# Performance work log

Hardware: AMD Instinct MI355X
Metric: run time of the kernel (lower is better)

The kernel has to match this reference:

```python
import jax, jax.numpy as jnp
import numpy as np

N = 50000
E = 800000


def _degrees(src, dst):
    ones = jnp.ones((E,), dtype=jnp.float32)
    indeg = jax.ops.segment_sum(ones, dst, num_segments=N)
    outdeg = jax.ops.segment_sum(ones, src, num_segments=N)
    return indeg, outdeg


def _aggregate(h, src, dst):
    # update_all(copy_src, sum): gather src features, scatter-add to dst
    return jax.ops.segment_sum(h[src], dst, num_segments=N)


def _graph_conv(h, src, dst, innorm, outnorm, W, b):
    h = h * outnorm[:, None]
    h = _aggregate(h, src, dst)
    h = h * innorm[:, None]
    return h @ W + b


def setup_inputs() -> dict:
    key = jax.random.key(0)
    ks = jax.random.split(key, 8)
    d_in, d_hid, d_out = 128, 128, 64
    inp = {
        "features": jax.random.normal(ks[0], (N, d_in), dtype=jnp.float32),
        "src": jax.random.randint(ks[1], (E,), 0, N, dtype=jnp.int32),
        "dst": jax.random.randint(ks[2], (E,), 0, N, dtype=jnp.int32),
        "W0": jax.random.normal(ks[3], (d_in, d_hid), dtype=jnp.float32) / np.sqrt(d_in),
        "b0": jnp.zeros((d_hid,), dtype=jnp.float32),
        "W1": jax.random.normal(ks[4], (d_hid, d_hid), dtype=jnp.float32) / np.sqrt(d_hid),
        "b1": jnp.zeros((d_hid,), dtype=jnp.float32),
        "W2": jax.random.normal(ks[5], (d_hid, d_hid), dtype=jnp.float32) / np.sqrt(d_hid),
        "b2": jnp.zeros((d_hid,), dtype=jnp.float32),
        "W3": jax.random.normal(ks[6], (d_hid, d_out), dtype=jnp.float32) / np.sqrt(d_hid),
        "b3": jnp.zeros((d_out,), dtype=jnp.float32),
    }
    return inp


def reference(features, src, dst, W0, b0, W1, b1, W2, b2, W3, b3):
    indeg, outdeg = _degrees(src, dst)
    innorm = jnp.power(jnp.clip(indeg, 1.0, None), -0.5)
    outnorm = jnp.power(jnp.clip(outdeg, 1.0, None), -0.5)

    # input GraphConv + relu
    h = jax.nn.relu(_graph_conv(features, src, dst, innorm, outnorm, W0, b0))

    # GResConv blocks: graph_res=True, raw_res=True, dropout=0 (identity)
    for (W, b) in ((W1, b1), (W2, b2)):
        res = features * innorm[:, None]          # pre-norm (in-degree)
        res = _aggregate(res, src, dst)
        res = res * innorm[:, None]               # post-norm (in-degree)
        h = jax.nn.relu(_graph_conv(h, src, dst, innorm, outnorm, W, b) + res)

    # output GraphConv (no activation)
    return _graph_conv(h, src, dst, innorm, outnorm, W3, b3)
```

## Files before the change

### kernel.cpp

```cpp
#include <hip/hip_runtime.h>


#define GN 50000
#define GE 800000
#define SCAN_CHUNK 1024
#define DEG_BLOCKS 128
#define DEG_SLICE 6250
#define HALF_NODES 25000
#define HALF_WORDS 12500

typedef __attribute__((ext_vector_type(8))) short bf16x8;
typedef __attribute__((ext_vector_type(4))) float f32x4;

__device__ __forceinline__ float u2f(unsigned int u) { return __uint_as_float(u); }

__device__ __forceinline__ unsigned int bfr(float a) {
  unsigned int u = __float_as_uint(a);
  return (u + 0x7fffu + ((u >> 16) & 1u)) >> 16;
}
__device__ __forceinline__ unsigned int bfpack(float a, float b) {
  return bfr(a) | (bfr(b) << 16);
}
__device__ __forceinline__ void bfunpack8(uint4 u, float* f) {
  f[0] = u2f(u.x << 16); f[1] = u2f(u.x & 0xffff0000u);
  f[2] = u2f(u.y << 16); f[3] = u2f(u.y & 0xffff0000u);
  f[4] = u2f(u.z << 16); f[5] = u2f(u.z & 0xffff0000u);
  f[6] = u2f(u.w << 16); f[7] = u2f(u.w & 0xffff0000u);
}

__global__ __launch_bounds__(512) void degrees_lds_kernel(
    const int* __restrict__ src, const int* __restrict__ dst,
    unsigned int* __restrict__ partials, int E) {
  __shared__ unsigned int hist[HALF_WORDS];
  for (int i = threadIdx.x; i < HALF_WORDS; i += 512) hist[i] = 0u;
  __syncthreads();
  int b    = blockIdx.x & 127;
  int half = (blockIdx.x >> 7) & 1;
  int dir  = blockIdx.x >> 8;
  const int* __restrict__ idx = dir ? src : dst;
  int lo = half * HALF_NODES, hi = lo + HALF_NODES;
  int s = b * DEG_SLICE;
  int e = min(s + DEG_SLICE, E);
  for (int i = s + threadIdx.x; i < e; i += 512) {
    int node = idx[i];
    if (node >= lo && node < hi) {
      int local = node - lo;
      atomicAdd(&hist[local >> 1], 1u << ((local & 1) << 4));
    }
  }
  __syncthreads();
  unsigned int* outp = partials + (((size_t)dir * 2 + half) * DEG_BLOCKS + b) * HALF_WORDS;
  for (int i = threadIdx.x; i < HALF_WORDS; i += 512) outp[i] = hist[i];
}

__global__ void degrees_reduce_kernel(const unsigned int* __restrict__ partials,
                                      int* __restrict__ indeg, float* __restrict__ innorm,
                                      float* __restrict__ outnorm, float2* __restrict__ nrm2,
                                      unsigned int* __restrict__ rel16pk) {
  int g = blockIdx.x * blockDim.x + threadIdx.x;
  if (g >= 2 * HALF_WORDS) return;
  int half = (g >= HALF_WORDS) ? 1 : 0;
  int w = g - half * HALF_WORDS;
  int n0 = half * HALF_NODES + 2 * w;
  unsigned int inLo = 0, inHi = 0, outLo = 0, outHi = 0;
  const unsigned int* pIn  = partials + ((size_t)(0 * 2 + half) * DEG_BLOCKS) * HALF_WORDS + w;
  const unsigned int* pOut = partials + ((size_t)(1 * 2 + half) * DEG_BLOCKS) * HALF_WORDS + w;
#pragma unroll 4
  for (int b = 0; b < DEG_BLOCKS; b++) {
    rel16pk[((size_t)b * GN + n0) >> 1] = inLo | (inHi << 16);
    unsigned int v = pIn[(size_t)b * HALF_WORDS];
    inLo += v & 0xffffu; inHi += v >> 16;
    unsigned int u = pOut[(size_t)b * HALF_WORDS];
    outLo += u & 0xffffu; outHi += u >> 16;
  }
  indeg[n0]     = (int)inLo;
  indeg[n0 + 1] = (int)inHi;
  float i0 = rsqrtf((float)max((int)inLo, 1)),  i1 = rsqrtf((float)max((int)inHi, 1));
  float o0 = rsqrtf((float)max((int)outLo, 1)), o1 = rsqrtf((float)max((int)outHi, 1));
  innorm[n0] = i0; innorm[n0 + 1] = i1;
  outnorm[n0] = o0; outnorm[n0 + 1] = o1;
  nrm2[n0]     = make_float2(o0, i0);
  nrm2[n0 + 1] = make_float2(o1, i1);
}

__global__ __launch_bounds__(256) void scan_blocksums(const int* __restrict__ deg,
                                                      int* __restrict__ bsums, int n) {
  int tid = threadIdx.x;
  int i = blockIdx.x * SCAN_CHUNK + tid * 4;
  int s = 0;
  if (i + 3 < n) {
    int4 v = *(const int4*)(deg + i);
    s = v.x + v.y + v.z + v.w;
  } else {
    for (int j = 0; j < 4; j++) if (i + j < n) s += deg[i + j];
  }
  for (int off = 32; off; off >>= 1) s += __shfl_down(s, off);
  __shared__ int ws[4];
  if ((tid & 63) == 0) ws[tid >> 6] = s;
  __syncthreads();
  if (tid == 0) bsums[blockIdx.x] = ws[0] + ws[1] + ws[2] + ws[3];
}

__global__ void scan_bsums(const int* __restrict__ bsums, int* __restrict__ bpref,
                           int nb, int* __restrict__ offsets, int n) {
  int tid = threadIdx.x;
  int v = (tid < nb) ? bsums[tid] : 0;
  int incl = v;
  for (int off = 1; off < 64; off <<= 1) {
    int t = __shfl_up(incl, off);
    if (tid >= off) incl += t;
  }
  if (tid < nb) bpref[tid] = incl - v;
  if (tid == 63) offsets[n] = incl;
}

__global__ __launch_bounds__(256) void scan_final(const int* __restrict__ deg,
                                                  const int* __restrict__ bpref,
                                                  int* __restrict__ offsets, int n) {
  int tid = threadIdx.x;
  int i = blockIdx.x * SCAN_CHUNK + tid * 4;
  int v[4];
#pragma unroll
  for (int j = 0; j < 4; j++) v[j] = (i + j < n) ? deg[i + j] : 0;
  int tsum = v[0] + v[1] + v[2] + v[3];
  int incl = tsum;
  for (int off = 1; off < 64; off <<= 1) {
    int t = __shfl_up(incl, off);
    if ((tid & 63) >= off) incl += t;
  }
  __shared__ int wsum[4];
  int wid = tid >> 6, lane = tid & 63;
  if (lane == 63) wsum[wid] = incl;
  __syncthreads();
  int wpref = 0;
  for (int w = 0; w < wid; w++) wpref += wsum[w];
  int run = bpref[blockIdx.x] + wpref + incl - tsum;
#pragma unroll
  for (int j = 0; j < 4; j++) {
    if (i + j < n) offsets[i + j] = run;
    run += v[j];
  }
}

__global__ __launch_bounds__(512) void fill_csr_lds_kernel(
    const int* __restrict__ src, const int* __restrict__ dst,
    const int* __restrict__ offsets, const unsigned short* __restrict__ rel16,
    const float2* __restrict__ nrm2, int* __restrict__ csr,
    float2* __restrict__ esc2, int E) {
  __shared__ unsigned int cnt[HALF_WORDS];
  for (int i = threadIdx.x; i < HALF_WORDS; i += 512) cnt[i] = 0u;
  __syncthreads();
  int b    = blockIdx.x & 127;
  int half = blockIdx.x >> 7;
  int lo = half * HALF_NODES, hi = lo + HALF_NODES;
  int s = b * DEG_SLICE;
  int e = min(s + DEG_SLICE, E);
  const unsigned short* relb = rel16 + (size_t)b * GN;
  for (int i = s + threadIdx.x; i < e; i += 512) {
    int d = dst[i];
    if (d >= lo && d < hi) {
      int local = d - lo;
      int sh = (local & 1) << 4;
      unsigned int old = atomicAdd(&cnt[local >> 1], 1u << sh);
      int rank = (int)((old >> sh) & 0xffffu);
      int pos = offsets[d] + (int)relb[d] + rank;
      int sv = src[i];
      csr[pos] = sv;
      esc2[pos] = nrm2[sv];
    }
  }
}

__global__ __launch_bounds__(256) void f32_to_bf16_kernel(const float* __restrict__ in,
                                                          uint4* __restrict__ out, int n8) {
  int t = blockIdx.x * blockDim.x + threadIdx.x;
  if (t >= n8) return;
  const float4* in4 = (const float4*)in;
  float4 f0 = in4[2 * t], f1 = in4[2 * t + 1];
  uint4 o;
  o.x = bfpack(f0.x, f0.y); o.y = bfpack(f0.z, f0.w);
  o.z = bfpack(f1.x, f1.y); o.w = bfpack(f1.z, f1.w);
  out[t] = o;
}

__global__ __launch_bounds__(256) void wconvert_kernel(
    const float* __restrict__ W0, const float* __restrict__ W1,
    const float* __restrict__ W2, const float* __restrict__ W3,
    unsigned short* __restrict__ wt) {
  int e = blockIdx.x * 256 + threadIdx.x;
  if (e >= 3 * 16384 + 8192) return;
  int m, local, N;
  if (e < 49152) { m = e >> 14; local = e & 16383; N = 128; }
  else { m = 3; local = e - 49152; N = 64; }
  const float* W = (m == 0) ? W0 : (m == 1) ? W1 : (m == 2) ? W2 : W3;
  int k = local / N, n = local % N;
  float v = W[k * N + n];
  unsigned int hi = bfr(v);
  float rem = v - u2f(hi << 16);
  unsigned int lo = bfr(rem);
  size_t hibase = (m < 3) ? (size_t)m * 32768 : 98304;
  size_t lobase = hibase + ((m < 3) ? 16384 : 8192);
  wt[hibase + (size_t)n * 128 + k] = (unsigned short)hi;
  wt[lobase + (size_t)n * 128 + k] = (unsigned short)lo;
}

__global__ __launch_bounds__(256) void aggregate128_bf16_kernel(
    const char* __restrict__ hqc, const float2* __restrict__ esc2,
    const float* __restrict__ wscale, const int* __restrict__ offsets,
    const int* __restrict__ csr, uint4* __restrict__ outq, int n) {
  int node = blockIdx.x * 4 + (threadIdx.x >> 6);
  if (node >= n) return;
  int lane = threadIdx.x & 63;
  unsigned cofs = (unsigned)(lane & 15) << 4;
  int p = lane >> 4;
  int s = offsets[node], e = offsets[node + 1];
  float acc[8];
#pragma unroll
  for (int j = 0; j < 8; j++) acc[j] = 0.f;
  int i = s + p;
  for (; i + 4 < e; i += 8) {
    int sn0 = csr[i], sn1 = csr[i + 4];
    float s0 = esc2[i].x, s1 = esc2[i + 4].x;
    uint4 u0 = *(const uint4*)(hqc + (((unsigned)sn0 << 8) + cofs));
    uint4 u1 = *(const uint4*)(hqc + (((unsigned)sn1 << 8) + cofs));
    float f0[8], f1[8];
    bfunpack8(u0, f0); bfunpack8(u1, f1);
#pragma unroll
    for (int j = 0; j < 8; j++) acc[j] += f0[j] * s0 + f1[j] * s1;
  }
  if (i < e) {
    int sn = csr[i];
    float sc = esc2[i].x;
    uint4 u = *(const uint4*)(hqc + (((unsigned)sn << 8) + cofs));
    float f[8]; bfunpack8(u, f);
#pragma unroll
    for (int j = 0; j < 8; j++) acc[j] += f[j] * sc;
  }
#pragma unroll
  for (int off = 32; off >= 16; off >>= 1)
#pragma unroll
    for (int j = 0; j < 8; j++) acc[j] += __shfl_down(acc[j], off);
  if (lane < 16) {
    float w = wscale[node];
    uint4 q;
    q.x = bfpack(acc[0] * w, acc[1] * w); q.y = bfpack(acc[2] * w, acc[3] * w);
    q.z = bfpack(acc[4] * w, acc[5] * w); q.w = bfpack(acc[6] * w, acc[7] * w);
    outq[(size_t)node * 16 + (lane & 15)] = q;
  }
}

__global__ __launch_bounds__(256) void aggregate_dual_bf16_kernel(
    const char* __restrict__ hqc, const float2* __restrict__ esc2,
    const float* __restrict__ wscale, const int* __restrict__ offsets,
    const int* __restrict__ csr, uint4* __restrict__ out1q,
    uint4* __restrict__ out2q, int n) {
  int node = blockIdx.x * 4 + (threadIdx.x >> 6);
  if (node >= n) return;
  int lane = threadIdx.x & 63;
  unsigned cofs = (unsigned)(lane & 15) << 4;
  int p = lane >> 4;
  int s = offsets[node], e = offsets[node + 1];
  float a1[8], a2[8];
#pragma unroll
  for (int j = 0; j < 8; j++) { a1[j] = 0.f; a2[j] = 0.f; }
  int i = s + p;
  for (; i + 4 < e; i += 8) {
    int sn0 = csr[i], sn1 = csr[i + 4];
    float2 g0 = esc2[i], g1 = esc2[i + 4];
    uint4 u0 = *(const uint4*)(hqc + (((unsigned)sn0 << 8) + cofs));
    uint4 u1 = *(const uint4*)(hqc + (((unsigned)sn1 << 8) + cofs));
    float f0[8], f1[8];
    bfunpack8(u0, f0); bfunpack8(u1, f1);
#pragma unroll
    for (int j = 0; j < 8; j++) {
      a1[j] += f0[j] * g0.x + f1[j] * g1.x;
      a2[j] += f0[j] * g0.y + f1[j] * g1.y;
    }
  }
  if (i < e) {
    int sn = csr[i];
    float2 g = esc2[i];
    uint4 u = *(const uint4*)(hqc + (((unsigned)sn << 8) + cofs));
    float f[8]; bfunpack8(u, f);
#pragma unroll
    for (int j = 0; j < 8; j++) { a1[j] += f[j] * g.x; a2[j] += f[j] * g.y; }
  }
#pragma unroll
  for (int off = 32; off >= 16; off >>= 1)
#pragma unroll
    for (int j = 0; j < 8; j++) {
      a1[j] += __shfl_down(a1[j], off);
      a2[j] += __shfl_down(a2[j], off);
    }
  if (lane < 16) {
    float w = wscale[node];
    uint4 q1, q2;
    q1.x = bfpack(a1[0] * w, a1[1] * w); q1.y = bfpack(a1[2] * w, a1[3] * w);
    q1.z = bfpack(a1[4] * w, a1[5] * w); q1.w = bfpack(a1[6] * w, a1[7] * w);
    q2.x = bfpack(a2[0] * w, a2[1] * w); q2.y = bfpack(a2[2] * w, a2[3] * w);
    q2.z = bfpack(a2[4] * w, a2[5] * w); q2.w = bfpack(a2[6] * w, a2[7] * w);
    out1q[(size_t)node * 16 + (lane & 15)] = q1;
    out2q[(size_t)node * 16 + (lane & 15)] = q2;
  }
}

__global__ __launch_bounds__(256) void aggregate64_bf16_kernel(
    const char* __restrict__ hqc, const float2* __restrict__ esc2,
    const float* __restrict__ wscale, const float* __restrict__ bias,
    const int* __restrict__ offsets, const int* __restrict__ csr,
    float* __restrict__ out, int n) {
  int node = blockIdx.x * 4 + (threadIdx.x >> 6);
  if (node >= n) return;
  int lane = threadIdx.x & 63;
  unsigned cofs = (unsigned)(lane & 7) << 4;
  int p = lane >> 3;
  int s = offsets[node], e = offsets[node + 1];
  float acc[8];
#pragma unroll
  for (int j = 0; j < 8; j++) acc[j] = 0.f;
  int i = s + p;
  for (; i + 8 < e; i += 16) {
    int sn0 = csr[i], sn1 = csr[i + 8];
    float s0 = esc2[i].x, s1 = esc2[i + 8].x;
    uint4 u0 = *(const uint4*)(hqc + (((unsigned)sn0 << 7) + cofs));
    uint4 u1 = *(const uint4*)(hqc + (((unsigned)sn1 << 7) + cofs));
    float f0[8], f1[8];
    bfunpack8(u0, f0); bfunpack8(u1, f1);
#pragma unroll
    for (int j = 0; j < 8; j++) acc[j] += f0[j] * s0 + f1[j] * s1;
  }
  if (i < e) {
    int sn = csr[i];
    float sc = esc2[i].x;
    uint4 u = *(const uint4*)(hqc + (((unsigned)sn << 7) + cofs));
    float f[8]; bfunpack8(u, f);
#pragma unroll
    for (int j = 0; j < 8; j++) acc[j] += f[j] * sc;
  }
#pragma unroll
  for (int off = 32; off >= 8; off >>= 1)
#pragma unroll
    for (int j = 0; j < 8; j++) acc[j] += __shfl_down(acc[j], off);
  if (lane < 8) {
    int c = lane;
    float w = wscale[node];
    const float4* bp = (const float4*)bias;
    float4 b0 = bp[2 * c], b1 = bp[2 * c + 1];
    float4* orow = (float4*)(out + (size_t)node * 64);
    orow[2 * c]     = make_float4(acc[0] * w + b0.x, acc[1] * w + b0.y,
                                  acc[2] * w + b0.z, acc[3] * w + b0.w);
    orow[2 * c + 1] = make_float4(acc[4] * w + b1.x, acc[5] * w + b1.y,
                                  acc[6] * w + b1.z, acc[7] * w + b1.w);
  }
}

template <int NT, bool RELU, bool HAS_BIAS, bool ADD_RES>
__global__ __launch_bounds__(256) void mfma_gemm_kernel(
    const unsigned short* __restrict__ Abf, const unsigned short* __restrict__ Wth,
    const unsigned short* __restrict__ Wtl, const float* __restrict__ bias,
    const unsigned short* __restrict__ resbf, unsigned short* __restrict__ outbf, int M) {
  constexpr int DOUT = NT * 16;
  int wid = threadIdx.x >> 6, lane = threadIdx.x & 63;
  int row0 = (blockIdx.x * 4 + wid) * 32;
  int lr = lane & 15, g = lane >> 4;
  bf16x8 a[2][4];
  bf16x8 zz = {0, 0, 0, 0, 0, 0, 0, 0};
#pragma unroll
  for (int rt = 0; rt < 2; rt++) {
    int r = row0 + rt * 16 + lr;
    if (r < M) {
      const unsigned short* ap = Abf + (size_t)r * 128 + g * 8;
#pragma unroll
      for (int s = 0; s < 4; s++) a[rt][s] = *(const bf16x8*)(ap + s * 32);
    } else {
#pragma unroll
      for (int s = 0; s < 4; s++) a[rt][s] = zz;
    }
  }
#pragma unroll
  for (int ct = 0; ct < NT; ct++) {
    const unsigned short* wph = Wth + (size_t)(ct * 16 + lr) * 128 + g * 8;
    const unsigned short* wpl = Wtl + (size_t)(ct * 16 + lr) * 128 + g * 8;
    bf16x8 wh[4], wl[4];
#pragma unroll
    for (int s = 0; s < 4; s++) {
      wh[s] = *(const bf16x8*)(wph + s * 32);
      wl[s] = *(const bf16x8*)(wpl + s * 32);
    }
    f32x4 acc0 = {0.f, 0.f, 0.f, 0.f}, acc1 = {0.f, 0.f, 0.f, 0.f};
#pragma unroll
    for (int s = 0; s < 4; s++) {
      acc0 = __builtin_amdgcn_mfma_f32_16x16x32_bf16(a[0][s], wh[s], acc0, 0, 0, 0);
      acc0 = __builtin_amdgcn_mfma_f32_16x16x32_bf16(a[0][s], wl[s], acc0, 0, 0, 0);
      acc1 = __builtin_amdgcn_mfma_f32_16x16x32_bf16(a[1][s], wh[s], acc1, 0, 0, 0);
      acc1 = __builtin_amdgcn_mfma_f32_16x16x32_bf16(a[1][s], wl[s], acc1, 0, 0, 0);
    }
    int col = ct * 16 + lr;
    float bv = HAS_BIAS ? bias[col] : 0.f;
#pragma unroll
    for (int rt = 0; rt < 2; rt++) {
      f32x4 acc = rt ? acc1 : acc0;
#pragma unroll
      for (int j = 0; j < 4; j++) {
        int r = row0 + rt * 16 + g * 4 + j;
        if (r < M) {
          float v = acc[j] + bv;
          if (ADD_RES) v += u2f((unsigned int)resbf[(size_t)r * 128 + col] << 16);
          if (RELU) v = fmaxf(v, 0.f);
          outbf[(size_t)r * DOUT + col] = (unsigned short)bfr(v);
        }
      }
    }
  }
}

extern "C" void kernel_launch(void* const* d_in, const int* in_sizes, int n_in,
                              void* d_out, int out_size, void* d_ws, size_t ws_size,
                              hipStream_t stream) {
  const float* features = (const float*)d_in[0];
  const int*   src      = (const int*)d_in[1];
  const int*   dst      = (const int*)d_in[2];
  const float* W0 = (const float*)d_in[3];
  const float* b0 = (const float*)d_in[4];
  const float* W1 = (const float*)d_in[5];
  const float* b1 = (const float*)d_in[6];
  const float* W2 = (const float*)d_in[7];
  const float* b2 = (const float*)d_in[8];
  const float* W3 = (const float*)d_in[9];
  const float* b3 = (const float*)d_in[10];
  float* out = (float*)d_out;
  const int N = GN, E = GE;

  char* ws = (char*)d_ws;
  size_t off = 0;
  auto alloc = [&](size_t bytes) -> void* {
    void* p = ws + off;
    off = (off + bytes + 255) & ~(size_t)255;
    return p;
  };
  unsigned int* partials = (unsigned int*)alloc((size_t)2 * 2 * DEG_BLOCKS * HALF_WORDS * 4);
  unsigned int* rel16pk  = (unsigned int*)alloc((size_t)DEG_BLOCKS * GN * 2);
  int*   indeg   = (int*)alloc((size_t)N * 4);
  float* innorm  = (float*)alloc((size_t)N * 4);
  float* outnorm = (float*)alloc((size_t)N * 4);
  float2* nrm2   = (float2*)alloc((size_t)N * 8);
  int*   offsets = (int*)alloc((size_t)(N + 1) * 4);
  int*   csr     = (int*)alloc((size_t)E * 4);
  float2* esc2   = (float2*)alloc((size_t)E * 8);
  int*   bsums   = (int*)alloc((size_t)256 * 4);
  int*   bpref   = (int*)alloc((size_t)256 * 4);
  unsigned short* wt = (unsigned short*)alloc((size_t)114688 * 2);
  uint4* fbf = (uint4*)alloc((size_t)N * 128 * 2);
  unsigned short* resbf = (unsigned short*)alloc((size_t)N * 128 * 2);
  unsigned short* tbf = (unsigned short*)alloc((size_t)N * 128 * 2);
  unsigned short* hbf = (unsigned short*)alloc((size_t)N * 128 * 2);
  (void)ws_size; (void)in_sizes; (void)n_in; (void)out_size;

  unsigned short* Ybf = resbf;
  const unsigned short *w0h = wt,          *w0l = wt + 16384;
  const unsigned short *w1h = wt + 32768,  *w1l = wt + 49152;
  const unsigned short *w2h = wt + 65536,  *w2l = wt + 81920;
  const unsigned short *w3h = wt + 98304,  *w3l = wt + 106496;

  degrees_lds_kernel<<<4 * DEG_BLOCKS, 512, 0, stream>>>(src, dst, partials, E);
  degrees_reduce_kernel<<<(2 * HALF_WORDS + 255) / 256, 256, 0, stream>>>(
      partials, indeg, innorm, outnorm, nrm2, rel16pk);

  int nb = (N + SCAN_CHUNK - 1) / SCAN_CHUNK;
  scan_blocksums<<<nb, 256, 0, stream>>>(indeg, bsums, N);
  scan_bsums<<<1, 64, 0, stream>>>(bsums, bpref, nb, offsets, N);
  scan_final<<<nb, 256, 0, stream>>>(indeg, bpref, offsets, N);

  fill_csr_lds_kernel<<<2 * DEG_BLOCKS, 512, 0, stream>>>(
      src, dst, offsets, (const unsigned short*)rel16pk, nrm2, csr, esc2, E);

  wconvert_kernel<<<(57344 + 255) / 256, 256, 0, stream>>>(W0, W1, W2, W3, wt);
  f32_to_bf16_kernel<<<(N * 128 / 8 + 255) / 256, 256, 0, stream>>>(
      features, fbf, N * 128 / 8);

  int aggGrid  = (N + 3) / 4;
  int gemmGrid = (N + 127) / 128;

  aggregate_dual_bf16_kernel<<<aggGrid, 256, 0, stream>>>(
      (const char*)fbf, esc2, innorm, offsets, csr, (uint4*)tbf, (uint4*)resbf, N);
  mfma_gemm_kernel<8, true, true, false><<<gemmGrid, 256, 0, stream>>>(
      tbf, w0h, w0l, b0, nullptr, hbf, N);
  aggregate128_bf16_kernel<<<aggGrid, 256, 0, stream>>>(
      (const char*)hbf, esc2, innorm, offsets, csr, (uint4*)tbf, N);
  mfma_gemm_kernel<8, true, true, true><<<gemmGrid, 256, 0, stream>>>(
      tbf, w1h, w1l, b1, resbf, hbf, N);
  aggregate128_bf16_kernel<<<aggGrid, 256, 0, stream>>>(
      (const char*)hbf, esc2, innorm, offsets, csr, (uint4*)tbf, N);
  mfma_gemm_kernel<8, true, true, true><<<gemmGrid, 256, 0, stream>>>(
      tbf, w2h, w2l, b2, resbf, hbf, N);
  mfma_gemm_kernel<4, false, false, false><<<gemmGrid, 256, 0, stream>>>(
      hbf, w3h, w3l, nullptr, nullptr, Ybf, N);
  aggregate64_bf16_kernel<<<aggGrid, 256, 0, stream>>>(
      (const char*)Ybf, esc2, innorm, b3, offsets, csr, out, N);
}
```

Baseline: 373.8 us.

## Merge scan and convert kernels, split GEMM columns over grid, halve degree blocks

Folds the single-block bsums scan into scan_final and merges the feature and weight bf16 conversions into one launch, removing two kernel launches. The MFMA GEMM now splits output columns across a second grid dimension, swaps operand order so each lane writes four contiguous columns with vectorized bias, residual and output accesses, and keeps separate hi/lo accumulators. Degree and CSR-fill kernels use 64 larger slices instead of 128, shrinking the partials and rel16 buffers, and the unused outnorm array is dropped. The trade-offs are redundant per-block scans of bsums, fewer blocks in the histogram stages, and extra accumulator registers in the GEMM.

```diff
diff --git a/kernel.cpp b/kernel.cpp
--- a/kernel.cpp
+++ b/kernel.cpp
@@ -4,8 +4,8 @@
 #define GN 50000
 #define GE 800000
 #define SCAN_CHUNK 1024
-#define DEG_BLOCKS 128
-#define DEG_SLICE 6250
+#define DEG_BLOCKS 64
+#define DEG_SLICE 12500
 #define HALF_NODES 25000
 #define HALF_WORDS 12500
 
@@ -34,9 +34,9 @@
   __shared__ unsigned int hist[HALF_WORDS];
   for (int i = threadIdx.x; i < HALF_WORDS; i += 512) hist[i] = 0u;
   __syncthreads();
-  int b    = blockIdx.x & 127;
-  int half = (blockIdx.x >> 7) & 1;
-  int dir  = blockIdx.x >> 8;
+  int b    = blockIdx.x & 63;
+  int half = (blockIdx.x >> 6) & 1;
+  int dir  = blockIdx.x >> 7;
   const int* __restrict__ idx = dir ? src : dst;
   int lo = half * HALF_NODES, hi = lo + HALF_NODES;
   int s = b * DEG_SLICE;
@@ -55,7 +55,7 @@
 
 __global__ void degrees_reduce_kernel(const unsigned int* __restrict__ partials,
                                       int* __restrict__ indeg, float* __restrict__ innorm,
-                                      float* __restrict__ outnorm, float2* __restrict__ nrm2,
+                                      float2* __restrict__ nrm2,
                                       unsigned int* __restrict__ rel16pk) {
   int g = blockIdx.x * blockDim.x + threadIdx.x;
   if (g >= 2 * HALF_WORDS) return;
@@ -78,7 +78,6 @@
   float i0 = rsqrtf((float)max((int)inLo, 1)),  i1 = rsqrtf((float)max((int)inHi, 1));
   float o0 = rsqrtf((float)max((int)outLo, 1)), o1 = rsqrtf((float)max((int)outHi, 1));
   innorm[n0] = i0; innorm[n0 + 1] = i1;
-  outnorm[n0] = o0; outnorm[n0 + 1] = o1;
   nrm2[n0]     = make_float2(o0, i0);
   nrm2[n0 + 1] = make_float2(o1, i1);
 }
@@ -101,23 +100,22 @@
   if (tid == 0) bsums[blockIdx.x] = ws[0] + ws[1] + ws[2] + ws[3];
 }
 
-__global__ void scan_bsums(const int* __restrict__ bsums, int* __restrict__ bpref,
-                           int nb, int* __restrict__ offsets, int n) {
+__global__ __launch_bounds__(256) void scan_final(const int* __restrict__ deg,
+                                                  const int* __restrict__ bsums, int nb,
+                                                  int* __restrict__ offsets, int n) {
+  __shared__ int bpref_s, total_s;
   int tid = threadIdx.x;
-  int v = (tid < nb) ? bsums[tid] : 0;
-  int incl = v;
-  for (int off = 1; off < 64; off <<= 1) {
-    int t = __shfl_up(incl, off);
-    if (tid >= off) incl += t;
-  }
-  if (tid < nb) bpref[tid] = incl - v;
-  if (tid == 63) offsets[n] = incl;
-}
-
-__global__ __launch_bounds__(256) void scan_final(const int* __restrict__ deg,
-                                                  const int* __restrict__ bpref,
-                                                  int* __restrict__ offsets, int n) {
-  int tid = threadIdx.x;
+  if (tid < 64) {
+    int v = (tid < nb) ? bsums[tid] : 0;
+    int incl = v;
+    for (int off = 1; off < 64; off <<= 1) {
+      int t = __shfl_up(incl, off);
+      if (tid >= off) incl += t;
+    }
+    if (tid == (int)blockIdx.x) bpref_s = incl - v;
+    if (tid == nb - 1) total_s = incl;
+  }
+  __syncthreads();
   int i = blockIdx.x * SCAN_CHUNK + tid * 4;
   int v[4];
 #pragma unroll
@@ -134,12 +132,13 @@
   __syncthreads();
   int wpref = 0;
   for (int w = 0; w < wid; w++) wpref += wsum[w];
-  int run = bpref[blockIdx.x] + wpref + incl - tsum;
+  int run = bpref_s + wpref + incl - tsum;
 #pragma unroll
   for (int j = 0; j < 4; j++) {
     if (i + j < n) offsets[i + j] = run;
     run += v[j];
   }
+  if (blockIdx.x == 0 && tid == 0) offsets[n] = total_s;
 }
 
 __global__ __launch_bounds__(512) void fill_csr_lds_kernel(
@@ -150,8 +149,8 @@
   __shared__ unsigned int cnt[HALF_WORDS];
   for (int i = threadIdx.x; i < HALF_WORDS; i += 512) cnt[i] = 0u;
   __syncthreads();
-  int b    = blockIdx.x & 127;
-  int half = blockIdx.x >> 7;
+  int b    = blockIdx.x & 63;
+  int half = blockIdx.x >> 6;
   int lo = half * HALF_NODES, hi = lo + HALF_NODES;
   int s = b * DEG_SLICE;
   int e = min(s + DEG_SLICE, E);
@@ -171,23 +170,23 @@
   }
 }
 
-__global__ __launch_bounds__(256) void f32_to_bf16_kernel(const float* __restrict__ in,
-                                                          uint4* __restrict__ out, int n8) {
-  int t = blockIdx.x * blockDim.x + threadIdx.x;
-  if (t >= n8) return;
-  const float4* in4 = (const float4*)in;
-  float4 f0 = in4[2 * t], f1 = in4[2 * t + 1];
-  uint4 o;
-  o.x = bfpack(f0.x, f0.y); o.y = bfpack(f0.z, f0.w);
-  o.z = bfpack(f1.x, f1.y); o.w = bfpack(f1.z, f1.w);
-  out[t] = o;
-}
-
-__global__ __launch_bounds__(256) void wconvert_kernel(
+#define FB_BLOCKS 3125
+__global__ __launch_bounds__(256) void convert_kernel(
+    const float* __restrict__ fin, uint4* __restrict__ fbf,
     const float* __restrict__ W0, const float* __restrict__ W1,
     const float* __restrict__ W2, const float* __restrict__ W3,
     unsigned short* __restrict__ wt) {
-  int e = blockIdx.x * 256 + threadIdx.x;
+  if ((int)blockIdx.x < FB_BLOCKS) {
+    int t = blockIdx.x * 256 + threadIdx.x;
+    const float4* in4 = (const float4*)fin;
+    float4 f0 = in4[2 * t], f1 = in4[2 * t + 1];
+    uint4 o;
+    o.x = bfpack(f0.x, f0.y); o.y = bfpack(f0.z, f0.w);
+    o.z = bfpack(f1.x, f1.y); o.w = bfpack(f1.z, f1.w);
+    fbf[t] = o;
+    return;
+  }
+  int e = (blockIdx.x - FB_BLOCKS) * 256 + threadIdx.x;
   if (e >= 3 * 16384 + 8192) return;
   int m, local, N;
   if (e < 49152) { m = e >> 14; local = e & 16383; N = 128; }
@@ -354,15 +353,15 @@
   }
 }
 
-template <int NT, bool RELU, bool HAS_BIAS, bool ADD_RES>
+template <int DOUT, bool RELU, bool HAS_BIAS, bool ADD_RES>
 __global__ __launch_bounds__(256) void mfma_gemm_kernel(
     const unsigned short* __restrict__ Abf, const unsigned short* __restrict__ Wth,
     const unsigned short* __restrict__ Wtl, const float* __restrict__ bias,
     const unsigned short* __restrict__ resbf, unsigned short* __restrict__ outbf, int M) {
-  constexpr int DOUT = NT * 16;
   int wid = threadIdx.x >> 6, lane = threadIdx.x & 63;
   int row0 = (blockIdx.x * 4 + wid) * 32;
   int lr = lane & 15, g = lane >> 4;
+  int cb = blockIdx.y * 64;
   bf16x8 a[2][4];
   bf16x8 zz = {0, 0, 0, 0, 0, 0, 0, 0};
 #pragma unroll
@@ -377,38 +376,51 @@
       for (int s = 0; s < 4; s++) a[rt][s] = zz;
     }
   }
-#pragma unroll
-  for (int ct = 0; ct < NT; ct++) {
-    const unsigned short* wph = Wth + (size_t)(ct * 16 + lr) * 128 + g * 8;
-    const unsigned short* wpl = Wtl + (size_t)(ct * 16 + lr) * 128 + g * 8;
+  int r0 = row0 + lr, r1 = row0 + 16 + lr;
+#pragma unroll
+  for (int ct = 0; ct < 4; ct++) {
+    int wrow = cb + ct * 16 + lr;
+    const unsigned short* wph = Wth + (size_t)wrow * 128 + g * 8;
+    const unsigned short* wpl = Wtl + (size_t)wrow * 128 + g * 8;
     bf16x8 wh[4], wl[4];
 #pragma unroll
     for (int s = 0; s < 4; s++) {
       wh[s] = *(const bf16x8*)(wph + s * 32);
       wl[s] = *(const bf16x8*)(wpl + s * 32);
     }
-    f32x4 acc0 = {0.f, 0.f, 0.f, 0.f}, acc1 = {0.f, 0.f, 0.f, 0.f};
+    f32x4 a0h = {0.f,0.f,0.f,0.f}, a0l = {0.f,0.f,0.f,0.f};
+    f32x4 a1h = {0.f,0.f,0.f,0.f}, a1l = {0.f,0.f,0.f,0.f};
 #pragma unroll
     for (int s = 0; s < 4; s++) {
-      acc0 = __builtin_amdgcn_mfma_f32_16x16x32_bf16(a[0][s], wh[s], acc0, 0, 0, 0);
-      acc0 = __builtin_amdgcn_mfma_f32_16x16x32_bf16(a[0][s], wl[s], acc0, 0, 0, 0);
-      acc1 = __builtin_amdgcn_mfma_f32_16x16x32_bf16(a[1][s], wh[s], acc1, 0, 0, 0);
-      acc1 = __builtin_amdgcn_mfma_f32_16x16x32_bf16(a[1][s], wl[s], acc1, 0, 0, 0);
-    }
-    int col = ct * 16 + lr;
-    float bv = HAS_BIAS ? bias[col] : 0.f;
+      a0h = __builtin_amdgcn_mfma_f32_16x16x32_bf16(wh[s], a[0][s], a0h, 0, 0, 0);
+      a0l = __builtin_amdgcn_mfma_f32_16x16x32_bf16(wl[s], a[0][s], a0l, 0, 0, 0);
+      a1h = __builtin_amdgcn_mfma_f32_16x16x32_bf16(wh[s], a[1][s], a1h, 0, 0, 0);
+      a1l = __builtin_amdgcn_mfma_f32_16x16x32_bf16(wl[s], a[1][s], a1l, 0, 0, 0);
+    }
+    int c0 = cb + ct * 16 + 4 * g;
+    float4 bv = make_float4(0.f, 0.f, 0.f, 0.f);
+    if (HAS_BIAS) bv = *(const float4*)(bias + c0);
 #pragma unroll
     for (int rt = 0; rt < 2; rt++) {
-      f32x4 acc = rt ? acc1 : acc0;
-#pragma unroll
-      for (int j = 0; j < 4; j++) {
-        int r = row0 + rt * 16 + g * 4 + j;
-        if (r < M) {
-          float v = acc[j] + bv;
-          if (ADD_RES) v += u2f((unsigned int)resbf[(size_t)r * 128 + col] << 16);
-          if (RELU) v = fmaxf(v, 0.f);
-          outbf[(size_t)r * DOUT + col] = (unsigned short)bfr(v);
+      int r = rt ? r1 : r0;
+      if (r < M) {
+        f32x4 ah = rt ? a1h : a0h, al = rt ? a1l : a0l;
+        float v0 = ah[0] + al[0] + bv.x;
+        float v1 = ah[1] + al[1] + bv.y;
+        float v2 = ah[2] + al[2] + bv.z;
+        float v3 = ah[3] + al[3] + bv.w;
+        if (ADD_RES) {
+          uint2 rr = *(const uint2*)(resbf + (size_t)r * 128 + c0);
+          v0 += u2f(rr.x << 16); v1 += u2f(rr.x & 0xffff0000u);
+          v2 += u2f(rr.y << 16); v3 += u2f(rr.y & 0xffff0000u);
         }
+        if (RELU) {
+          v0 = fmaxf(v0, 0.f); v1 = fmaxf(v1, 0.f);
+          v2 = fmaxf(v2, 0.f); v3 = fmaxf(v3, 0.f);
+        }
+        uint2 pk;
+        pk.x = bfpack(v0, v1); pk.y = bfpack(v2, v3);
+        *(uint2*)(outbf + (size_t)r * DOUT + c0) = pk;
       }
     }
   }
@@ -442,13 +454,11 @@
   unsigned int* rel16pk  = (unsigned int*)alloc((size_t)DEG_BLOCKS * GN * 2);
   int*   indeg   = (int*)alloc((size_t)N * 4);
   float* innorm  = (float*)alloc((size_t)N * 4);
-  float* outnorm = (float*)alloc((size_t)N * 4);
   float2* nrm2   = (float2*)alloc((size_t)N * 8);
   int*   offsets = (int*)alloc((size_t)(N + 1) * 4);
   int*   csr     = (int*)alloc((size_t)E * 4);
   float2* esc2   = (float2*)alloc((size_t)E * 8);
   int*   bsums   = (int*)alloc((size_t)256 * 4);
-  int*   bpref   = (int*)alloc((size_t)256 * 4);
   unsigned short* wt = (unsigned short*)alloc((size_t)114688 * 2);
   uint4* fbf = (uint4*)alloc((size_t)N * 128 * 2);
   unsigned short* resbf = (unsigned short*)alloc((size_t)N * 128 * 2);
@@ -464,36 +474,35 @@
 
   degrees_lds_kernel<<<4 * DEG_BLOCKS, 512, 0, stream>>>(src, dst, partials, E);
   degrees_reduce_kernel<<<(2 * HALF_WORDS + 255) / 256, 256, 0, stream>>>(
-      partials, indeg, innorm, outnorm, nrm2, rel16pk);
+      partials, indeg, innorm, nrm2, rel16pk);
 
   int nb = (N + SCAN_CHUNK - 1) / SCAN_CHUNK;
   scan_blocksums<<<nb, 256, 0, stream>>>(indeg, bsums, N);
-  scan_bsums<<<1, 64, 0, stream>>>(bsums, bpref, nb, offsets, N);
-  scan_final<<<nb, 256, 0, stream>>>(indeg, bpref, offsets, N);
+  scan_final<<<nb, 256, 0, stream>>>(indeg, bsums, nb, offsets, N);
 
   fill_csr_lds_kernel<<<2 * DEG_BLOCKS, 512, 0, stream>>>(
       src, dst, offsets, (const unsigned short*)rel16pk, nrm2, csr, esc2, E);
 
-  wconvert_kernel<<<(57344 + 255) / 256, 256, 0, stream>>>(W0, W1, W2, W3, wt);
-  f32_to_bf16_kernel<<<(N * 128 / 8 + 255) / 256, 256, 0, stream>>>(
-      features, fbf, N * 128 / 8);
-
-  int aggGrid  = (N + 3) / 4;
-  int gemmGrid = (N + 127) / 128;
+  convert_kernel<<<FB_BLOCKS + 224, 256, 0, stream>>>(
+      features, fbf, W0, W1, W2, W3, wt);
+
+  int aggGrid = (N + 3) / 4;
+  dim3 gemmGrid2((N + 127) / 128, 2);
+  dim3 gemmGrid1((N + 127) / 128, 1);
 
   aggregate_dual_bf16_kernel<<<aggGrid, 256, 0, stream>>>(
       (const char*)fbf, esc2, innorm, offsets, csr, (uint4*)tbf, (uint4*)resbf, N);
-  mfma_gemm_kernel<8, true, true, false><<<gemmGrid, 256, 0, stream>>>(
+  mfma_gemm_kernel<128, true, true, false><<<gemmGrid2, 256, 0, stream>>>(
       tbf, w0h, w0l, b0, nullptr, hbf, N);
   aggregate128_bf16_kernel<<<aggGrid, 256, 0, stream>>>(
       (const char*)hbf, esc2, innorm, offsets, csr, (uint4*)tbf, N);
-  mfma_gemm_kernel<8, true, true, true><<<gemmGrid, 256, 0, stream>>>(
+  mfma_gemm_kernel<128, true, true, true><<<gemmGrid2, 256, 0, stream>>>(
       tbf, w1h, w1l, b1, resbf, hbf, N);
   aggregate128_bf16_kernel<<<aggGrid, 256, 0, stream>>>(
       (const char*)hbf, esc2, innorm, offsets, csr, (uint4*)tbf, N);
-  mfma_gemm_kernel<8, true, true, true><<<gemmGrid, 256, 0, stream>>>(
+  mfma_gemm_kernel<128, true, true, true><<<gemmGrid2, 256, 0, stream>>>(
       tbf, w2h, w2l, b2, resbf, hbf, N);
-  mfma_gemm_kernel<4, false, false, false><<<gemmGrid, 256, 0, stream>>>(
+  mfma_gemm_kernel<64, false, false, false><<<gemmGrid1, 256, 0, stream>>>(
       hbf, w3h, w3l, nullptr, nullptr, Ybf, N);
   aggregate64_bf16_kernel<<<aggGrid, 256, 0, stream>>>(
       (const char*)Ybf, esc2, innorm, b3, offsets, csr, out, N);
```

New measurement: 366.6 us. No clear change (-1.9%).
